# Kernel optimization log

Measured on AMD Instinct MI355X. Metric: run time of the kernel, lower is better.

Reference implementation:

```python
import jax, jax.numpy as jnp
import numpy as np

D_MODEL = 1024
NHEAD = 16
HEAD_DIM = D_MODEL // NHEAD


def setup_inputs() -> dict:
    key = jax.random.key(0)
    ks = jax.random.split(key, 11)
    B, S = 2, 2048
    s = 1.0 / np.sqrt(D_MODEL)
    return {
        "query": jax.random.normal(ks[0], (B, S, D_MODEL), jnp.float32),
        "key": jax.random.normal(ks[1], (B, S, D_MODEL), jnp.float32),
        "value": jax.random.normal(ks[2], (B, S, D_MODEL), jnp.float32),
        "wq_w": jax.random.normal(ks[3], (D_MODEL, D_MODEL), jnp.float32) * s,
        "wq_b": jax.random.normal(ks[4], (D_MODEL,), jnp.float32) * s,
        "wk_w": jax.random.normal(ks[5], (D_MODEL, D_MODEL), jnp.float32) * s,
        "wk_b": jax.random.normal(ks[6], (D_MODEL,), jnp.float32) * s,
        "wv_w": jax.random.normal(ks[7], (D_MODEL, D_MODEL), jnp.float32) * s,
        "wv_b": jax.random.normal(ks[8], (D_MODEL,), jnp.float32) * s,
        "wo_w": jax.random.normal(ks[9], (D_MODEL, D_MODEL), jnp.float32) * s,
        "wo_b": jax.random.normal(ks[10], (D_MODEL,), jnp.float32) * s,
    }


def reference(query, key, value, wq_w, wq_b, wk_w, wk_b, wv_w, wv_b, wo_w, wo_b):
    B, S, _ = query.shape
    # torch Linear: x @ W.T + b
    def proj(x, w, b):
        y = x @ w.T + b
        return y.reshape(B, S, NHEAD, HEAD_DIM).transpose(0, 2, 1, 3)  # [B,H,S,Dh]

    Q = proj(query, wq_w, wq_b)
    K = proj(key, wk_w, wk_b)
    V = proj(value, wv_w, wv_b)

    scale = 1.0 / np.sqrt(HEAD_DIM).astype(np.float32)
    scores = jnp.einsum("bhqd,bhkd->bhqk", Q, K) * scale  # [B,H,S,S]
    causal = jnp.tril(jnp.ones((S, S), dtype=bool))
    scores = jnp.where(causal, scores, -jnp.inf)
    attn = jax.nn.softmax(scores, axis=-1)
    out = jnp.einsum("bhqk,bhkd->bhqd", attn, V)  # [B,H,S,Dh]
    out = out.transpose(0, 2, 1, 3).reshape(B, S, D_MODEL)
    return out @ wo_w.T + wo_b
```

## Files before the change

### kernel.cpp

```cpp
#include <hip/hip_runtime.h>
#include <stdint.h>

#define D_MODEL 1024
#define S_LEN   2048
#define NHEAD   16
#define HEAD_DIM 64
#define BATCH   2
#define M_TOT   (BATCH * S_LEN)
#define Q_SCALE 0.18033688011112042f

using bf16x8 = __attribute__((ext_vector_type(8))) short;
using f32x4  = __attribute__((ext_vector_type(4))) float;

__device__ __forceinline__ float bf2f(unsigned short h) {
  union { unsigned int u; float f; } v; v.u = ((unsigned int)h) << 16; return v.f;
}
__device__ __forceinline__ unsigned short f2bf(float f) {
  union { float f; unsigned int u; } v; v.f = f;
  unsigned int u = v.u;
  return (unsigned short)((u + 0x7FFFu + ((u >> 16) & 1u)) >> 16);
}
__device__ __forceinline__ unsigned int pkbf(float a, float b) {
#if __has_builtin(__builtin_amdgcn_cvt_pk_bf16_f32)
  auto p = __builtin_amdgcn_cvt_pk_bf16_f32(a, b);
  union { decltype(p) v; unsigned int u; } c; c.v = p;
  return c.u;
#else
  return (unsigned int)f2bf(a) | ((unsigned int)f2bf(b) << 16);
#endif
}
__device__ __forceinline__ bf16x8 cvt8(const float* p) {
  const float4 a = *(const float4*)p;
  const float4 b = *(const float4*)(p + 4);
  union { unsigned int u[4]; bf16x8 v; } r;
  r.u[0] = pkbf(a.x, a.y); r.u[1] = pkbf(a.z, a.w);
  r.u[2] = pkbf(b.x, b.y); r.u[3] = pkbf(b.z, b.w);
  return r.v;
}
__device__ __forceinline__ float fexp2(float x) {
#if __has_builtin(__builtin_amdgcn_exp2f)
  return __builtin_amdgcn_exp2f(x);
#else
  return __expf(x * 0.69314718055994531f);
#endif
}

#define LDK 40

__global__ __launch_bounds__(256)
void cast_weights(const float* __restrict__ wq, const float* __restrict__ wk,
                  const float* __restrict__ wv, const float* __restrict__ wo,
                  unsigned short* __restrict__ dst)
{
  const int z = blockIdx.y;
  const float* src = (z == 0) ? wq : (z == 1) ? wk : (z == 2) ? wv : wo;
  unsigned short* d = dst + (size_t)z * D_MODEL * D_MODEL;
  const size_t i = ((size_t)blockIdx.x * 256 + threadIdx.x) * 8;
  *(bf16x8*)(d + i) = cvt8(src + i);
}

template<bool AF32>
__device__ __forceinline__ void gemm_tile(const void* __restrict__ Av,
                                          const unsigned short* __restrict__ W,
                                          int m0, int n0,
                                          short* As, short* Bs,
                                          f32x4 acc[4][4])
{
  const int t    = threadIdx.x;
  const int lane = t & 63;
  const int w    = t >> 6;
  const int quad = lane >> 4;
  const int l16  = lane & 15;
  const int wm   = (w >> 1) * 64;
  const int wn   = (w & 1) * 64;
  const int srow = t >> 2;
  const int scol = (t & 3) * 8;

  for (int mt = 0; mt < 4; ++mt)
    for (int nt = 0; nt < 4; ++nt)
      acc[mt][nt] = f32x4{0.f, 0.f, 0.f, 0.f};

  for (int kt = 0; kt < D_MODEL / 32; ++kt) {
    const int kc = kt * 32 + scol;
    bf16x8 a0, a1;
    if (AF32) {
      const float* A = (const float*)Av;
      a0 = cvt8(A + (size_t)(m0 + srow)      * D_MODEL + kc);
      a1 = cvt8(A + (size_t)(m0 + srow + 64) * D_MODEL + kc);
    } else {
      const unsigned short* A = (const unsigned short*)Av;
      a0 = *(const bf16x8*)(A + (size_t)(m0 + srow)      * D_MODEL + kc);
      a1 = *(const bf16x8*)(A + (size_t)(m0 + srow + 64) * D_MODEL + kc);
    }
    const bf16x8 b0 = *(const bf16x8*)(W + (size_t)(n0 + srow)      * D_MODEL + kc);
    const bf16x8 b1 = *(const bf16x8*)(W + (size_t)(n0 + srow + 64) * D_MODEL + kc);
    __syncthreads();
    *(bf16x8*)(As + (srow)      * LDK + scol) = a0;
    *(bf16x8*)(As + (srow + 64) * LDK + scol) = a1;
    *(bf16x8*)(Bs + (srow)      * LDK + scol) = b0;
    *(bf16x8*)(Bs + (srow + 64) * LDK + scol) = b1;
    __syncthreads();

    bf16x8 af[4], bfr[4];
    for (int mt = 0; mt < 4; ++mt)
      af[mt] = *(const bf16x8*)(As + (wm + mt * 16 + l16) * LDK + quad * 8);
    for (int nt = 0; nt < 4; ++nt)
      bfr[nt] = *(const bf16x8*)(Bs + (wn + nt * 16 + l16) * LDK + quad * 8);
    for (int mt = 0; mt < 4; ++mt)
      for (int nt = 0; nt < 4; ++nt)
        acc[mt][nt] = __builtin_amdgcn_mfma_f32_16x16x32_bf16(af[mt], bfr[nt], acc[mt][nt], 0, 0, 0);
  }
}

__global__ __launch_bounds__(256)
void qkv_proj(const float* __restrict__ query,
              const float* __restrict__ key,
              const float* __restrict__ value,
              const unsigned short* __restrict__ wqb,
              const unsigned short* __restrict__ wkb,
              const unsigned short* __restrict__ wvb,
              const float* __restrict__ bq,
              const float* __restrict__ bk,
              const float* __restrict__ bv,
              unsigned short* __restrict__ Qh,
              unsigned short* __restrict__ Kh,
              unsigned short* __restrict__ VhT)
{
  __shared__ __attribute__((aligned(16))) short As[128 * LDK];
  __shared__ __attribute__((aligned(16))) short Bs[128 * LDK];
  const int z = blockIdx.z;
  const float*          A    = (z == 0) ? query : (z == 1) ? key : value;
  const unsigned short* W    = (z == 0) ? wqb   : (z == 1) ? wkb : wvb;
  const float*          bias = (z == 0) ? bq    : (z == 1) ? bk  : bv;
  unsigned short*       dst  = (z == 0) ? Qh    : (z == 1) ? Kh  : VhT;
  const float           scale = (z == 0) ? Q_SCALE : 1.0f;

  const int m0 = blockIdx.x * 128;
  const int n0 = blockIdx.y * 128;
  f32x4 acc[4][4];
  gemm_tile<true>(A, W, m0, n0, As, Bs, acc);

  const int t    = threadIdx.x;
  const int lane = t & 63;
  const int w    = t >> 6;
  const int quad = lane >> 4;
  const int l16  = lane & 15;
  const int wm   = (w >> 1) * 64;
  const int wn   = (w & 1) * 64;

  for (int nt = 0; nt < 4; ++nt) {
    const int n = n0 + wn + nt * 16 + l16;
    const float bb = bias[n];
    const int h = n >> 6, d = n & 63;
    for (int mt = 0; mt < 4; ++mt) {
      for (int r = 0; r < 4; ++r) {
        const int m = m0 + wm + mt * 16 + quad * 4 + r;
        const int b = m >> 11, s = m & 2047;
        const unsigned short val = f2bf((acc[mt][nt][r] + bb) * scale);
        if (z < 2)
          dst[((size_t)((b * NHEAD + h) * S_LEN + s)) * HEAD_DIM + d] = val;
        else
          dst[((size_t)((b * NHEAD + h) * HEAD_DIM + d)) * S_LEN + s] = val;
      }
    }
  }
}

__global__ __launch_bounds__(256)
void out_proj(const unsigned short* __restrict__ Oh,
              const unsigned short* __restrict__ wob,
              const float* __restrict__ bo,
              float* __restrict__ dst)
{
  __shared__ __attribute__((aligned(16))) short As[128 * LDK];
  __shared__ __attribute__((aligned(16))) short Bs[128 * LDK];
  const int m0 = blockIdx.x * 128;
  const int n0 = blockIdx.y * 128;
  f32x4 acc[4][4];
  gemm_tile<false>(Oh, wob, m0, n0, As, Bs, acc);

  const int t    = threadIdx.x;
  const int lane = t & 63;
  const int w    = t >> 6;
  const int quad = lane >> 4;
  const int l16  = lane & 15;
  const int wm   = (w >> 1) * 64;
  const int wn   = (w & 1) * 64;

  for (int nt = 0; nt < 4; ++nt) {
    const int n = n0 + wn + nt * 16 + l16;
    const float bb = bo[n];
    for (int mt = 0; mt < 4; ++mt) {
      for (int r = 0; r < 4; ++r) {
        const int m = m0 + wm + mt * 16 + quad * 4 + r;
        dst[(size_t)m * D_MODEL + n] = acc[mt][nt][r] + bb;
      }
    }
  }
}

__global__ __launch_bounds__(256)
void attn_kernel(const unsigned short* __restrict__ Qh,
                 const unsigned short* __restrict__ Kh,
                 const unsigned short* __restrict__ VhT,
                 unsigned short* __restrict__ O)
{
  __shared__ __attribute__((aligned(16))) short Ks[128 * 72];
  __shared__ __attribute__((aligned(16))) short Vts[64 * 136];
  __shared__ __attribute__((aligned(16))) short Ps[4][16 * 136];

  const int bh   = blockIdx.x;
  const int qt   = (int)gridDim.y - 1 - (int)blockIdx.y;
  const int q0   = qt * 64;
  const int b    = bh >> 4;
  const int h    = bh & 15;
  const int t    = threadIdx.x;
  const int w    = t >> 6;
  const int lane = t & 63;
  const int quad = lane >> 4;
  const int l16  = lane & 15;
  const size_t headK = (size_t)bh * S_LEN * HEAD_DIM;
  const size_t headV = (size_t)bh * HEAD_DIM * S_LEN;

  bf16x8 qf[2];
  {
    const size_t qrow = (size_t)bh * S_LEN + (q0 + w * 16 + l16);
    qf[0] = *(const bf16x8*)(Qh + qrow * HEAD_DIM + quad * 8);
    qf[1] = *(const bf16x8*)(Qh + qrow * HEAD_DIM + 32 + quad * 8);
  }
  bf16x8 ones;
  for (int j = 0; j < 8; ++j) ones[j] = (short)0x3F80;

  float m_r[4] = {-INFINITY, -INFINITY, -INFINITY, -INFINITY};
  float l_r[4] = {0.f, 0.f, 0.f, 0.f};
  f32x4 oacc[4];
  for (int dt = 0; dt < 4; ++dt) oacc[dt] = f32x4{0.f, 0.f, 0.f, 0.f};

  const int rowbase = q0 + w * 16;
  const int rowmax  = rowbase + 15;
  const int kr = t >> 3, kc = (t & 7) * 8;
  const int vd = t >> 4, vc = (t & 15) * 8;

  const int nkt = (qt + 2) >> 1;
  for (int kt = 0; kt < nkt; ++kt) {
    const int k0 = kt * 128;
    __syncthreads();
    for (int i = 0; i < 4; ++i) {
      const int rr = kr + i * 32;
      *(bf16x8*)(Ks + rr * 72 + kc) =
          *(const bf16x8*)(Kh + headK + (size_t)(k0 + rr) * HEAD_DIM + kc);
      const int dd = vd + i * 16;
      *(bf16x8*)(Vts + dd * 136 + vc) =
          *(const bf16x8*)(VhT + headV + (size_t)dd * S_LEN + k0 + vc);
    }
    __syncthreads();

    float st[8][4];
    for (int nt = 0; nt < 8; ++nt) {
      const int c0 = k0 + nt * 16;
      if (c0 <= rowmax) {
        f32x4 s = f32x4{0.f, 0.f, 0.f, 0.f};
        for (int ks = 0; ks < 2; ++ks) {
          const bf16x8 kf = *(const bf16x8*)(Ks + (nt * 16 + l16) * 72 + ks * 32 + quad * 8);
          s = __builtin_amdgcn_mfma_f32_16x16x32_bf16(qf[ks], kf, s, 0, 0, 0);
        }
        if (c0 + 15 <= rowbase) {
          for (int r = 0; r < 4; ++r) st[nt][r] = s[r];
        } else {
          const int colg = c0 + l16;
          for (int r = 0; r < 4; ++r) {
            const int rowg = rowbase + quad * 4 + r;
            st[nt][r] = (colg <= rowg) ? s[r] : -INFINITY;
          }
        }
      } else {
        for (int r = 0; r < 4; ++r) st[nt][r] = -INFINITY;
      }
    }

    float alpha[4];
    for (int r = 0; r < 4; ++r) {
      float mx = st[0][r];
      for (int nt = 1; nt < 8; ++nt) mx = fmaxf(mx, st[nt][r]);
      for (int off = 1; off < 16; off <<= 1) mx = fmaxf(mx, __shfl_xor(mx, off));
      const float mn = fmaxf(m_r[r], mx);
      alpha[r] = fexp2(m_r[r] - mn);
      m_r[r] = mn;
      for (int nt = 0; nt < 8; ++nt) st[nt][r] = fexp2(st[nt][r] - mn);
    }
    for (int nt = 0; nt < 8; nt += 2) {
      for (int r = 0; r < 4; ++r) {
        const unsigned int u = pkbf(st[nt][r], st[nt + 1][r]);
        short* base = &Ps[w][(quad * 4 + r) * 136 + nt * 16 + l16];
        base[0]  = (short)(u & 0xffffu);
        base[16] = (short)(u >> 16);
      }
    }

    for (int dt = 0; dt < 4; ++dt)
      for (int r = 0; r < 4; ++r) oacc[dt][r] *= alpha[r];

    f32x4 lsum = f32x4{0.f, 0.f, 0.f, 0.f};
    for (int ks = 0; ks < 4; ++ks) {
      if (k0 + ks * 32 > rowmax) break;
      const bf16x8 pf = *(const bf16x8*)(&Ps[w][0] + l16 * 136 + ks * 32 + quad * 8);
      lsum = __builtin_amdgcn_mfma_f32_16x16x32_bf16(pf, ones, lsum, 0, 0, 0);
      for (int dt = 0; dt < 4; ++dt) {
        const bf16x8 vf = *(const bf16x8*)(Vts + (dt * 16 + l16) * 136 + ks * 32 + quad * 8);
        oacc[dt] = __builtin_amdgcn_mfma_f32_16x16x32_bf16(pf, vf, oacc[dt], 0, 0, 0);
      }
    }
    for (int r = 0; r < 4; ++r) l_r[r] = l_r[r] * alpha[r] + lsum[r];
  }

  for (int dt = 0; dt < 4; ++dt) {
    for (int r = 0; r < 4; ++r) {
      const int rowg = q0 + w * 16 + quad * 4 + r;
      O[(size_t)(b * S_LEN + rowg) * D_MODEL + h * 64 + dt * 16 + l16] =
          f2bf(oacc[dt][r] / l_r[r]);
    }
  }
}

extern "C" void kernel_launch(void* const* d_in, const int* in_sizes, int n_in,
                              void* d_out, int out_size, void* d_ws, size_t ws_size,
                              hipStream_t stream)
{
  (void)in_sizes; (void)n_in; (void)out_size; (void)ws_size;
  const float* q  = (const float*)d_in[0];
  const float* k  = (const float*)d_in[1];
  const float* v  = (const float*)d_in[2];
  const float* wq = (const float*)d_in[3];
  const float* bq = (const float*)d_in[4];
  const float* wk = (const float*)d_in[5];
  const float* bk = (const float*)d_in[6];
  const float* wv = (const float*)d_in[7];
  const float* bv = (const float*)d_in[8];
  const float* wo = (const float*)d_in[9];
  const float* bo = (const float*)d_in[10];
  float* out = (float*)d_out;

  unsigned short* wb  = (unsigned short*)d_ws;
  unsigned short* wqb = wb;
  unsigned short* wkb = wb + (size_t)1 * D_MODEL * D_MODEL;
  unsigned short* wvb = wb + (size_t)2 * D_MODEL * D_MODEL;
  unsigned short* wob = wb + (size_t)3 * D_MODEL * D_MODEL;
  unsigned short* Kh  = wb + (size_t)4 * D_MODEL * D_MODEL;
  unsigned short* VhT = Kh + (size_t)M_TOT * D_MODEL;
  unsigned short* Oh  = VhT + (size_t)M_TOT * D_MODEL;
  unsigned short* Qh  = (unsigned short*)d_out;

  dim3 g0(D_MODEL * D_MODEL / (256 * 8), 4, 1);
  cast_weights<<<g0, 256, 0, stream>>>(wq, wk, wv, wo, wb);

  dim3 g1(M_TOT / 128, D_MODEL / 128, 3);
  qkv_proj<<<g1, 256, 0, stream>>>(q, k, v, wqb, wkb, wvb, bq, bk, bv, Qh, Kh, VhT);

  dim3 g2(BATCH * NHEAD, S_LEN / 64, 1);
  attn_kernel<<<g2, 256, 0, stream>>>(Qh, Kh, VhT, Oh);

  dim3 g3(M_TOT / 128, D_MODEL / 128, 1);
  out_proj<<<g3, 256, 0, stream>>>(Oh, wob, bo, out);
}
```

Baseline: 236.5 us.

## Pre-cast activations to bf16 and stream GEMM tiles with direct global-to-LDS loads

Adds a kernel that converts query, key and value to bf16 into spare workspace and output buffers. The QKV and output projections then load A and W tiles through global_load_lds straight into unpadded shared memory, so the fp32-to-bf16 conversion and the register staging no longer sit inside the GEMM main loop. The new path runs only when the workspace is at least 40 MB; otherwise the old fp32-input kernel is used. The cost is an extra full read and write of the activations, plus likely LDS bank conflicts from the unpadded 32-element rows.

```diff
diff --git a/kernel.cpp b/kernel.cpp
--- a/kernel.cpp
+++ b/kernel.cpp
@@ -44,6 +44,14 @@
   return __expf(x * 0.69314718055994531f);
 #endif
 }
+__device__ __forceinline__ void async16(const unsigned short* g, short* l) {
+  __builtin_amdgcn_global_load_lds(
+      reinterpret_cast<const __attribute__((address_space(1))) unsigned int*>(
+          reinterpret_cast<uintptr_t>(g)),
+      reinterpret_cast<__attribute__((address_space(3))) unsigned int*>(
+          reinterpret_cast<uintptr_t>(l)),
+      16, 0, 0);
+}
 
 #define LDK 40
 
@@ -59,12 +67,64 @@
   *(bf16x8*)(d + i) = cvt8(src + i);
 }
 
-template<bool AF32>
-__device__ __forceinline__ void gemm_tile(const void* __restrict__ Av,
-                                          const unsigned short* __restrict__ W,
-                                          int m0, int n0,
-                                          short* As, short* Bs,
-                                          f32x4 acc[4][4])
+__global__ __launch_bounds__(256)
+void cast_inputs(const float* __restrict__ q, const float* __restrict__ k,
+                 const float* __restrict__ v,
+                 unsigned short* __restrict__ qb, unsigned short* __restrict__ kb,
+                 unsigned short* __restrict__ vb)
+{
+  const int z = blockIdx.y;
+  const float* src = (z == 0) ? q : (z == 1) ? k : v;
+  unsigned short* d = (z == 0) ? qb : (z == 1) ? kb : vb;
+  const size_t i = ((size_t)blockIdx.x * 256 + threadIdx.x) * 8;
+  *(bf16x8*)(d + i) = cvt8(src + i);
+}
+
+__device__ __forceinline__ void gemm_tile_lds(const unsigned short* __restrict__ A,
+                                              const unsigned short* __restrict__ W,
+                                              int m0, int n0,
+                                              short* As, short* Bs,
+                                              f32x4 acc[4][4])
+{
+  const int t    = threadIdx.x;
+  const int lane = t & 63;
+  const int w    = t >> 6;
+  const int quad = lane >> 4;
+  const int l16  = lane & 15;
+  const int wm   = (w >> 1) * 64;
+  const int wn   = (w & 1) * 64;
+  const int srow = w * 16 + (lane >> 2);
+  const int scol = (lane & 3) * 8;
+
+  for (int mt = 0; mt < 4; ++mt)
+    for (int nt = 0; nt < 4; ++nt)
+      acc[mt][nt] = f32x4{0.f, 0.f, 0.f, 0.f};
+
+  for (int kt = 0; kt < D_MODEL / 32; ++kt) {
+    const int kc = kt * 32 + scol;
+    __syncthreads();
+    async16(A + (size_t)(m0 + srow)      * D_MODEL + kc, As + srow * 32 + scol);
+    async16(A + (size_t)(m0 + 64 + srow) * D_MODEL + kc, As + (64 + srow) * 32 + scol);
+    async16(W + (size_t)(n0 + srow)      * D_MODEL + kc, Bs + srow * 32 + scol);
+    async16(W + (size_t)(n0 + 64 + srow) * D_MODEL + kc, Bs + (64 + srow) * 32 + scol);
+    __syncthreads();
+
+    bf16x8 af[4], bfr[4];
+    for (int mt = 0; mt < 4; ++mt)
+      af[mt] = *(const bf16x8*)(As + (wm + mt * 16 + l16) * 32 + quad * 8);
+    for (int nt = 0; nt < 4; ++nt)
+      bfr[nt] = *(const bf16x8*)(Bs + (wn + nt * 16 + l16) * 32 + quad * 8);
+    for (int mt = 0; mt < 4; ++mt)
+      for (int nt = 0; nt < 4; ++nt)
+        acc[mt][nt] = __builtin_amdgcn_mfma_f32_16x16x32_bf16(af[mt], bfr[nt], acc[mt][nt], 0, 0, 0);
+  }
+}
+
+__device__ __forceinline__ void gemm_tile_f32(const float* __restrict__ A,
+                                              const unsigned short* __restrict__ W,
+                                              int m0, int n0,
+                                              short* As, short* Bs,
+                                              f32x4 acc[4][4])
 {
   const int t    = threadIdx.x;
   const int lane = t & 63;
@@ -82,16 +142,8 @@
 
   for (int kt = 0; kt < D_MODEL / 32; ++kt) {
     const int kc = kt * 32 + scol;
-    bf16x8 a0, a1;
-    if (AF32) {
-      const float* A = (const float*)Av;
-      a0 = cvt8(A + (size_t)(m0 + srow)      * D_MODEL + kc);
-      a1 = cvt8(A + (size_t)(m0 + srow + 64) * D_MODEL + kc);
-    } else {
-      const unsigned short* A = (const unsigned short*)Av;
-      a0 = *(const bf16x8*)(A + (size_t)(m0 + srow)      * D_MODEL + kc);
-      a1 = *(const bf16x8*)(A + (size_t)(m0 + srow + 64) * D_MODEL + kc);
-    }
+    const bf16x8 a0 = cvt8(A + (size_t)(m0 + srow)      * D_MODEL + kc);
+    const bf16x8 a1 = cvt8(A + (size_t)(m0 + srow + 64) * D_MODEL + kc);
     const bf16x8 b0 = *(const bf16x8*)(W + (size_t)(n0 + srow)      * D_MODEL + kc);
     const bf16x8 b1 = *(const bf16x8*)(W + (size_t)(n0 + srow + 64) * D_MODEL + kc);
     __syncthreads();
@@ -112,34 +164,12 @@
   }
 }
 
-__global__ __launch_bounds__(256)
-void qkv_proj(const float* __restrict__ query,
-              const float* __restrict__ key,
-              const float* __restrict__ value,
-              const unsigned short* __restrict__ wqb,
-              const unsigned short* __restrict__ wkb,
-              const unsigned short* __restrict__ wvb,
-              const float* __restrict__ bq,
-              const float* __restrict__ bk,
-              const float* __restrict__ bv,
-              unsigned short* __restrict__ Qh,
-              unsigned short* __restrict__ Kh,
-              unsigned short* __restrict__ VhT)
-{
-  __shared__ __attribute__((aligned(16))) short As[128 * LDK];
-  __shared__ __attribute__((aligned(16))) short Bs[128 * LDK];
-  const int z = blockIdx.z;
-  const float*          A    = (z == 0) ? query : (z == 1) ? key : value;
-  const unsigned short* W    = (z == 0) ? wqb   : (z == 1) ? wkb : wvb;
-  const float*          bias = (z == 0) ? bq    : (z == 1) ? bk  : bv;
-  unsigned short*       dst  = (z == 0) ? Qh    : (z == 1) ? Kh  : VhT;
-  const float           scale = (z == 0) ? Q_SCALE : 1.0f;
-
-  const int m0 = blockIdx.x * 128;
-  const int n0 = blockIdx.y * 128;
-  f32x4 acc[4][4];
-  gemm_tile<true>(A, W, m0, n0, As, Bs, acc);
-
+__device__ __forceinline__ void qkv_epilogue(int z, int m0, int n0,
+                                             const float* __restrict__ bias,
+                                             float scale,
+                                             unsigned short* __restrict__ dst,
+                                             f32x4 acc[4][4])
+{
   const int t    = threadIdx.x;
   const int lane = t & 63;
   const int w    = t >> 6;
@@ -167,17 +197,69 @@
 }
 
 __global__ __launch_bounds__(256)
+void qkv_fast(const unsigned short* __restrict__ qb,
+              const unsigned short* __restrict__ kb,
+              const unsigned short* __restrict__ vb,
+              const unsigned short* __restrict__ wqb,
+              const unsigned short* __restrict__ wkb,
+              const unsigned short* __restrict__ wvb,
+              const float* __restrict__ bq, const float* __restrict__ bk,
+              const float* __restrict__ bv,
+              unsigned short* __restrict__ Qh, unsigned short* __restrict__ Kh,
+              unsigned short* __restrict__ VhT)
+{
+  __shared__ __attribute__((aligned(16))) short As[128 * 32];
+  __shared__ __attribute__((aligned(16))) short Bs[128 * 32];
+  const int z = blockIdx.z;
+  const unsigned short* A    = (z == 0) ? qb  : (z == 1) ? kb  : vb;
+  const unsigned short* W    = (z == 0) ? wqb : (z == 1) ? wkb : wvb;
+  const float*          bias = (z == 0) ? bq  : (z == 1) ? bk  : bv;
+  unsigned short*       dst  = (z == 0) ? Qh  : (z == 1) ? Kh  : VhT;
+  const float           scale = (z == 0) ? Q_SCALE : 1.0f;
+
+  const int m0 = blockIdx.x * 128, n0 = blockIdx.y * 128;
+  f32x4 acc[4][4];
+  gemm_tile_lds(A, W, m0, n0, As, Bs, acc);
+  qkv_epilogue(z, m0, n0, bias, scale, dst, acc);
+}
+
+__global__ __launch_bounds__(256)
+void qkv_slow(const float* __restrict__ query, const float* __restrict__ key,
+              const float* __restrict__ value,
+              const unsigned short* __restrict__ wqb,
+              const unsigned short* __restrict__ wkb,
+              const unsigned short* __restrict__ wvb,
+              const float* __restrict__ bq, const float* __restrict__ bk,
+              const float* __restrict__ bv,
+              unsigned short* __restrict__ Qh, unsigned short* __restrict__ Kh,
+              unsigned short* __restrict__ VhT)
+{
+  __shared__ __attribute__((aligned(16))) short As[128 * LDK];
+  __shared__ __attribute__((aligned(16))) short Bs[128 * LDK];
+  const int z = blockIdx.z;
+  const float*          A    = (z == 0) ? query : (z == 1) ? key : value;
+  const unsigned short* W    = (z == 0) ? wqb   : (z == 1) ? wkb : wvb;
+  const float*          bias = (z == 0) ? bq    : (z == 1) ? bk  : bv;
+  unsigned short*       dst  = (z == 0) ? Qh    : (z == 1) ? Kh  : VhT;
+  const float           scale = (z == 0) ? Q_SCALE : 1.0f;
+
+  const int m0 = blockIdx.x * 128, n0 = blockIdx.y * 128;
+  f32x4 acc[4][4];
+  gemm_tile_f32(A, W, m0, n0, As, Bs, acc);
+  qkv_epilogue(z, m0, n0, bias, scale, dst, acc);
+}
+
+__global__ __launch_bounds__(256)
 void out_proj(const unsigned short* __restrict__ Oh,
               const unsigned short* __restrict__ wob,
               const float* __restrict__ bo,
               float* __restrict__ dst)
 {
-  __shared__ __attribute__((aligned(16))) short As[128 * LDK];
-  __shared__ __attribute__((aligned(16))) short Bs[128 * LDK];
-  const int m0 = blockIdx.x * 128;
-  const int n0 = blockIdx.y * 128;
+  __shared__ __attribute__((aligned(16))) short As[128 * 32];
+  __shared__ __attribute__((aligned(16))) short Bs[128 * 32];
+  const int m0 = blockIdx.x * 128, n0 = blockIdx.y * 128;
   f32x4 acc[4][4];
-  gemm_tile<false>(Oh, wob, m0, n0, As, Bs, acc);
+  gemm_tile_lds(Oh, wob, m0, n0, As, Bs, acc);
 
   const int t    = threadIdx.x;
   const int lane = t & 63;
@@ -190,12 +272,11 @@
   for (int nt = 0; nt < 4; ++nt) {
     const int n = n0 + wn + nt * 16 + l16;
     const float bb = bo[n];
-    for (int mt = 0; mt < 4; ++mt) {
+    for (int mt = 0; mt < 4; ++mt)
       for (int r = 0; r < 4; ++r) {
         const int m = m0 + wm + mt * 16 + quad * 4 + r;
         dst[(size_t)m * D_MODEL + n] = acc[mt][nt][r] + bb;
       }
-    }
   }
 }
 
@@ -326,7 +407,7 @@
                               void* d_out, int out_size, void* d_ws, size_t ws_size,
                               hipStream_t stream)
 {
-  (void)in_sizes; (void)n_in; (void)out_size; (void)ws_size;
+  (void)in_sizes; (void)n_in; (void)out_size;
   const float* q  = (const float*)d_in[0];
   const float* k  = (const float*)d_in[1];
   const float* v  = (const float*)d_in[2];
@@ -348,13 +429,24 @@
   unsigned short* Kh  = wb + (size_t)4 * D_MODEL * D_MODEL;
   unsigned short* VhT = Kh + (size_t)M_TOT * D_MODEL;
   unsigned short* Oh  = VhT + (size_t)M_TOT * D_MODEL;
+  unsigned short* qb  = Oh;
+  unsigned short* vb  = Oh + (size_t)M_TOT * D_MODEL;
   unsigned short* Qh  = (unsigned short*)d_out;
+  unsigned short* kb  = Qh + (size_t)M_TOT * D_MODEL;
+
+  const bool fast = ws_size >= (size_t)40 * 1024 * 1024;
 
   dim3 g0(D_MODEL * D_MODEL / (256 * 8), 4, 1);
   cast_weights<<<g0, 256, 0, stream>>>(wq, wk, wv, wo, wb);
 
   dim3 g1(M_TOT / 128, D_MODEL / 128, 3);
-  qkv_proj<<<g1, 256, 0, stream>>>(q, k, v, wqb, wkb, wvb, bq, bk, bv, Qh, Kh, VhT);
+  if (fast) {
+    dim3 gc((size_t)M_TOT * D_MODEL / (256 * 8), 3, 1);
+    cast_inputs<<<gc, 256, 0, stream>>>(q, k, v, qb, kb, vb);
+    qkv_fast<<<g1, 256, 0, stream>>>(qb, kb, vb, wqb, wkb, wvb, bq, bk, bv, Qh, Kh, VhT);
+  } else {
+    qkv_slow<<<g1, 256, 0, stream>>>(q, k, v, wqb, wkb, wvb, bq, bk, bv, Qh, Kh, VhT);
+  }
 
   dim3 g2(BATCH * NHEAD, S_LEN / 64, 1);
   attn_kernel<<<g2, 256, 0, stream>>>(Qh, Kh, VhT, Oh);
```

Result: no change. 232.8 us (-1.5%).
